# Kernel optimization log

Measured on AMD Instinct MI355X. Metric: run time of the kernel, lower is better.

## Reference

```python
import jax, jax.numpy as jnp
import numpy as np

# Structure matrix S (n_hos*n_types=6, n_structures=8) and internal int_S (unused in forward)
S_MAT = np.array([[1,0,1,0,0,1,0,1],[0,1,0,1,1,0,0,0],[1,1,0,0,0,0,1,0],[0,0,1,1,0,1,0,0],[0,1,1,0,1,0,0,1],[1,0,0,0,1,0,1,0]], dtype=np.float32)
CONTROL_STRENGTH = 10.0  # self.control_strength
PDHG_ITERS = 150         # fixed-iteration batched primal-dual LP solver
BATCH = 32768
N_STRUCT = 8
N_COMBO = 6


def setup_inputs() -> dict:
    key = jax.random.key(0)
    ks = jax.random.split(key, 9)
    X = jax.random.uniform(ks[0], (BATCH, 2, 3), jnp.float32)  # nonnegative bids
    def lin(k, fan_in, fan_out):
        return jax.random.normal(k, (fan_in, fan_out), jnp.float32) * (1.0 / np.sqrt(fan_in))
    W1 = lin(ks[1], 6, 20);  b1 = jnp.zeros((20,), jnp.float32)
    W2 = lin(ks[2], 20, 20); b2 = jnp.zeros((20,), jnp.float32)
    W3 = lin(ks[3], 20, 20); b3 = jnp.zeros((20,), jnp.float32)
    W4 = lin(ks[4], 20, 8);  b4 = jnp.zeros((8,), jnp.float32)
    S = jnp.asarray(S_MAT)
    return {"X": X, "W1": W1, "b1": b1, "W2": W2, "b2": b2, "W3": W3, "b3": b3,
            "W4": W4, "b4": b4, "S": S, "batch_size": BATCH}


def _mlp(Z, W1, b1, W2, b2, W3, b3, W4, b4):
    h = jnp.tanh(Z @ W1 + b1)
    h = jnp.tanh(h @ W2 + b2)
    h = jnp.tanh(h @ W3 + b3)
    return h @ W4 + b4  # [B, 8]


def _batched_lp(S, z, bvec):
    """Solve, per batch row: max 1'x - c*||x - z||_2  s.t. x>=0, S x <= b.
    Equivalent polytope A x <= b' with A=[S; -I], b'=[b; 0]; solved with PDHG.
    z, bvec: [B, 8], [B, 6]."""
    B = z.shape[0]
    A = jnp.concatenate([S, -jnp.eye(N_STRUCT, dtype=S.dtype)], axis=0)  # [14, 8]
    bfull = jnp.concatenate([bvec, jnp.zeros((B, N_STRUCT), bvec.dtype)], axis=1)  # [B, 14]
    L = jnp.linalg.norm(A)  # Frobenius norm upper-bounds spectral norm
    tau = 1.0 / L
    sigma = 1.0 / L

    def prox_g(v):
        # prox of g(x) = -1'x + c||x - z||_2 (w = ones): shift by tau*w then shrink toward z
        u = v + tau
        d = u - z
        n = jnp.linalg.norm(d, axis=-1, keepdims=True)
        scale = jnp.maximum(0.0, 1.0 - tau * CONTROL_STRENGTH / jnp.maximum(n, 1e-12))
        return z + scale * d

    x0 = jnp.maximum(z, 0.0)
    y0 = jnp.zeros((B, N_COMBO + N_STRUCT), z.dtype)

    def step(carry, _):
        x, xbar, y = carry
        y = jnp.maximum(0.0, y + sigma * (xbar @ A.T - bfull))  # dual ascent + proj >= 0
        x_new = prox_g(x - tau * (y @ A))                        # primal prox step
        return (x_new, 2.0 * x_new - x, y), None

    (x, _, _), _ = jax.lax.scan(step, (x0, x0, y0), None, length=PDHG_ITERS)
    return x


def reference(X, W1, b1, W2, b2, W3, b3, W4, b4, S, batch_size):
    B = X.shape[0]
    Z = X.reshape(B, N_COMBO)              # view(-1, n_hos*n_types)
    z = _mlp(Z, W1, b1, W2, b2, W3, b3, W4, b4)  # neural_net_forward -> [B, 8]
    x1 = _batched_lp(S, z, Z)              # linear_program_forward (W = ones)
    return x1
```

## Files before the change

### kernel.cpp

```cpp
#include <hip/hip_runtime.h>
#include <math.h>


#define N_ITERS 150
typedef float f2 __attribute__((ext_vector_type(2)));
typedef float f4 __attribute__((ext_vector_type(4)));

__device__ __forceinline__ float fast_tanh(float a) {
    float e = __expf(2.0f * a);
    return 1.0f - 2.0f * __builtin_amdgcn_rcpf(e + 1.0f);
}

__device__ __forceinline__ float dpp_swap(float v) {
    union { float f; int i; } u;
    u.f = v;
    u.i = __builtin_amdgcn_update_dpp(0, u.i, 0xB1, 0xF, 0xF, true);
    return u.f;
}

__global__ void __launch_bounds__(64)
__attribute__((amdgpu_waves_per_eu(1, 1)))
matchnet_kernel(
    const float* __restrict__ X,
    const float* __restrict__ W1, const float* __restrict__ b1,
    const float* __restrict__ W2, const float* __restrict__ b2,
    const float* __restrict__ W3, const float* __restrict__ b3,
    const float* __restrict__ W4, const float* __restrict__ b4,
    float* __restrict__ out, int B)
{
    __shared__ alignas(16) float tW1[160], tW2[400], tW3[400], tW4[160];
    __shared__ alignas(16) float sb1[20], sb2[20], sb3[20], sb4[8];
    {
        int tid = threadIdx.x;
        for (int idx = tid; idx < 120; idx += 64) { int i = idx / 20, j = idx % 20; tW1[j * 8 + i] = W1[idx]; }
        for (int idx = tid; idx < 400; idx += 64) { int i = idx / 20, j = idx % 20; tW2[j * 20 + i] = W2[idx]; }
        for (int idx = tid; idx < 400; idx += 64) { int i = idx / 20, j = idx % 20; tW3[j * 20 + i] = W3[idx]; }
        for (int idx = tid; idx < 160; idx += 64) { int i = idx / 8,  k = idx % 8;  tW4[k * 20 + i] = W4[idx]; }
        if (tid < 20) { sb1[tid] = b1[tid]; sb2[tid] = b2[tid]; sb3[tid] = b3[tid]; }
        if (tid < 8) sb4[tid] = b4[tid];
    }
    __syncthreads();

    int gidx = blockIdx.x * blockDim.x + threadIdx.x;
    int row = gidx >> 1;
    if (row >= B) return;
    const bool isOdd = (gidx & 1) != 0;
    const int jb = isOdd ? 10 : 0;
    const int kb = isOdd ? 4 : 0;

    float bb0 = X[row * 6 + 0], bb1 = X[row * 6 + 1], bb2 = X[row * 6 + 2];
    float bb3 = X[row * 6 + 3], bb4 = X[row * 6 + 4], bb5 = X[row * 6 + 5];

    float hA[10], hB[10];
    {
        float acc[10];
        const f2* bv = (const f2*)&sb1[jb];
        #pragma unroll
        for (int p = 0; p < 5; p++) { f2 b = bv[p]; acc[2 * p] = b.x; acc[2 * p + 1] = b.y; }
        #pragma unroll
        for (int n = 0; n < 10; n++) {
            int j = jb + n;
            f4 w0 = *(const f4*)&tW1[j * 8];
            f2 w1 = *(const f2*)&tW1[j * 8 + 4];
            float a = acc[n];
            a = fmaf(bb0, w0.x, a); a = fmaf(bb1, w0.y, a); a = fmaf(bb2, w0.z, a);
            a = fmaf(bb3, w0.w, a); a = fmaf(bb4, w1.x, a); a = fmaf(bb5, w1.y, a);
            acc[n] = fast_tanh(a);
        }
        #pragma unroll
        for (int n = 0; n < 10; n++) {
            float t = dpp_swap(acc[n]);
            hA[n] = isOdd ? t : acc[n];
            hB[n] = isOdd ? acc[n] : t;
        }
    }
    #pragma unroll
    for (int layer = 0; layer < 2; layer++) {
        const float* tw = layer ? tW3 : tW2;
        const float* sb = layer ? sb3 : sb2;
        float acc[10];
        const f2* bv = (const f2*)&sb[jb];
        #pragma unroll
        for (int p = 0; p < 5; p++) { f2 b = bv[p]; acc[2 * p] = b.x; acc[2 * p + 1] = b.y; }
        #pragma unroll
        for (int n = 0; n < 10; n++) {
            int j = jb + n;
            const f4* w = (const f4*)&tw[j * 20];
            f4 w0 = w[0], w1 = w[1], w2 = w[2], w3 = w[3], w4 = w[4];
            float a = acc[n];
            a = fmaf(hA[0], w0.x, a); a = fmaf(hA[1], w0.y, a);
            a = fmaf(hA[2], w0.z, a); a = fmaf(hA[3], w0.w, a);
            a = fmaf(hA[4], w1.x, a); a = fmaf(hA[5], w1.y, a);
            a = fmaf(hA[6], w1.z, a); a = fmaf(hA[7], w1.w, a);
            a = fmaf(hA[8], w2.x, a); a = fmaf(hA[9], w2.y, a);
            a = fmaf(hB[0], w2.z, a); a = fmaf(hB[1], w2.w, a);
            a = fmaf(hB[2], w3.x, a); a = fmaf(hB[3], w3.y, a);
            a = fmaf(hB[4], w3.z, a); a = fmaf(hB[5], w3.w, a);
            a = fmaf(hB[6], w4.x, a); a = fmaf(hB[7], w4.y, a);
            a = fmaf(hB[8], w4.z, a); a = fmaf(hB[9], w4.w, a);
            acc[n] = fast_tanh(a);
        }
        #pragma unroll
        for (int n = 0; n < 10; n++) {
            float t = dpp_swap(acc[n]);
            hA[n] = isOdd ? t : acc[n];
            hB[n] = isOdd ? acc[n] : t;
        }
    }
    float oz0, oz1, oz2, oz3;
    {
        f4 b = *(const f4*)&sb4[kb];
        float acc[4] = {b.x, b.y, b.z, b.w};
        #pragma unroll
        for (int n = 0; n < 4; n++) {
            int k = kb + n;
            const f4* w = (const f4*)&tW4[k * 20];
            f4 w0 = w[0], w1 = w[1], w2 = w[2], w3 = w[3], w4 = w[4];
            float a = acc[n];
            a = fmaf(hA[0], w0.x, a); a = fmaf(hA[1], w0.y, a);
            a = fmaf(hA[2], w0.z, a); a = fmaf(hA[3], w0.w, a);
            a = fmaf(hA[4], w1.x, a); a = fmaf(hA[5], w1.y, a);
            a = fmaf(hA[6], w1.z, a); a = fmaf(hA[7], w1.w, a);
            a = fmaf(hA[8], w2.x, a); a = fmaf(hA[9], w2.y, a);
            a = fmaf(hB[0], w2.z, a); a = fmaf(hB[1], w2.w, a);
            a = fmaf(hB[2], w3.x, a); a = fmaf(hB[3], w3.y, a);
            a = fmaf(hB[4], w3.z, a); a = fmaf(hB[5], w3.w, a);
            a = fmaf(hB[6], w4.x, a); a = fmaf(hB[7], w4.y, a);
            a = fmaf(hB[8], w4.z, a); a = fmaf(hB[9], w4.w, a);
            acc[n] = a;
        }
        oz0 = acc[0]; oz1 = acc[1]; oz2 = acc[2]; oz3 = acc[3];
    }

    const float tau  = 0.18898223650461363f;
    const float c    = 0.03571428571428571f;
    const float tauC = 1.8898223650461363f;

    float ot0 = tau - oz0, ot1 = tau - oz1, ot2 = tau - oz2, ot3 = tau - oz3;
    float oTI0 = ot0, oTI1 = ot1, oTI2 = ot2, oTI3 = ot3;

    float ox0 = fmaxf(oz0, 0.f), ox1 = fmaxf(oz1, 0.f);
    float ox2 = fmaxf(oz2, 0.f), ox3 = fmaxf(oz3, 0.f);
    float oxb0 = ox0, oxb1 = ox1, oxb2 = ox2, oxb3 = ox3;

    float cb0 = c * bb0, cb1 = c * bb1, cb2 = c * bb2;
    float cb3 = c * bb3, cb4 = c * bb4, cb5 = c * bb5;
    float cbq0 = isOdd ? cb4 : cb0;
    float cbq1 = isOdd ? cb3 : cb2;
    float cbq2 = isOdd ? cb5 : cb1;
    float Yq0 = 0.f, Yq1 = 0.f, Yq2 = 0.f;

    #pragma unroll 1
    for (int it = 0; it < N_ITERS; it++) {
        float rxb0 = dpp_swap(oxb0), rxb1 = dpp_swap(oxb1);
        float rxb2 = dpp_swap(oxb2), rxb3 = dpp_swap(oxb3);

        float op_a = oxb0 + rxb1;
        float op_b = oxb2 + rxb3;
        float op_c = oxb3 + rxb2;
        float op_d = isOdd ? op_c : op_b;
        float sq0  = op_a + op_d;
        float op_e = oxb1 + rxb2;
        float op_f = isOdd ? rxb3 : oxb0;
        float sq1  = op_e + op_f;
        float op_g = oxb1 + oxb3;
        float op_h = oxb0 + oxb2;
        float op_i = isOdd ? op_h : op_g;
        float sq2  = op_i + rxb0;

        Yq0 = fmaxf(0.f, fmaf(c, sq0, Yq0) - cbq0);
        Yq1 = fmaxf(0.f, fmaf(c, sq1, Yq1) - cbq1);
        Yq2 = fmaxf(0.f, fmaf(c, sq2, Yq2) - cbq2);

        float rY0 = dpp_swap(Yq0), rY1 = dpp_swap(Yq1), rY2 = dpp_swap(Yq2);

        float op_j = Yq0 + rY2;
        float op_k = isOdd ? Yq2 : Yq1;
        float colq0 = op_j + op_k;
        float op_l = Yq1 + rY0;
        float op_p = isOdd ? 0.f : Yq2;
        float colq1 = op_l + op_p;
        float op_m = Yq0 + rY0;
        float op_n = rY1 + Yq2;
        float op_o = op_m + rY1;
        float colq2 = isOdd ? op_n : op_o;
        float colq3 = isOdd ? op_m : op_n;

        oTI0 = fmaxf(ot0, fmaf(-c, oxb0, oTI0));
        oTI1 = fmaxf(ot1, fmaf(-c, oxb1, oTI1));
        oTI2 = fmaxf(ot2, fmaf(-c, oxb2, oTI2));
        oTI3 = fmaxf(ot3, fmaf(-c, oxb3, oTI3));

        float od0 = (ox0 + oTI0) - colq0;
        float od1 = (ox1 + oTI1) - colq1;
        float od2 = (ox2 + oTI2) - colq2;
        float od3 = (ox3 + oTI3) - colq3;

        float nl = od0 * od0;
        nl = fmaf(od1, od1, nl);
        nl = fmaf(od2, od2, nl);
        nl = fmaf(od3, od3, nl);
        float rn = dpp_swap(nl);
        float nsq = nl + rn;

        float rs = __builtin_amdgcn_rsqf(nsq);
        float scale = fmaxf(0.f, fmaf(-tauC, rs, 1.f));

        float xn0 = fmaf(scale, od0, oz0);
        float xn1 = fmaf(scale, od1, oz1);
        float xn2 = fmaf(scale, od2, oz2);
        float xn3 = fmaf(scale, od3, oz3);
        oxb0 = fmaf(2.f, xn0, -ox0); ox0 = xn0;
        oxb1 = fmaf(2.f, xn1, -ox1); ox1 = xn1;
        oxb2 = fmaf(2.f, xn2, -ox2); ox2 = xn2;
        oxb3 = fmaf(2.f, xn3, -ox3); ox3 = xn3;
    }

    float4* out4 = (float4*)out;
    out4[gidx] = make_float4(ox0, ox1, ox2, ox3);
}

extern "C" void kernel_launch(void* const* d_in, const int* in_sizes, int n_in,
                              void* d_out, int out_size, void* d_ws, size_t ws_size,
                              hipStream_t stream) {
    const float* X  = (const float*)d_in[0];
    const float* W1 = (const float*)d_in[1];
    const float* b1 = (const float*)d_in[2];
    const float* W2 = (const float*)d_in[3];
    const float* b2 = (const float*)d_in[4];
    const float* W3 = (const float*)d_in[5];
    const float* b3 = (const float*)d_in[6];
    const float* W4 = (const float*)d_in[7];
    const float* b4 = (const float*)d_in[8];
    float* out = (float*)d_out;

    int B = in_sizes[0] / 6;
    const int block = 64;
    long long threads = (long long)B * 2;
    int grid = (int)((threads + block - 1) / block);
    hipLaunchKernelGGL(matchnet_kernel, dim3(grid), dim3(block), 0, stream,
                       X, W1, b1, W2, b2, W3, b3, W4, b4, out, B);
}
```

Baseline: 101.6 us.

## Process one batch row per thread instead of splitting rows across lane pairs

Each thread now computes the full MLP and the full 8-variable PDHG iteration for one row, removing the DPP lane-swap exchanges and the row split across paired lanes. This eliminates the cross-lane communication and the redundant selects. In exchange it halves the number of threads and waves, so each thread carries twice the per-iteration work and fewer SIMDs are occupied.

```diff
diff --git a/kernel.cpp b/kernel.cpp
--- a/kernel.cpp
+++ b/kernel.cpp
@@ -9,13 +9,6 @@
 __device__ __forceinline__ float fast_tanh(float a) {
     float e = __expf(2.0f * a);
     return 1.0f - 2.0f * __builtin_amdgcn_rcpf(e + 1.0f);
-}
-
-__device__ __forceinline__ float dpp_swap(float v) {
-    union { float f; int i; } u;
-    u.f = v;
-    u.i = __builtin_amdgcn_update_dpp(0, u.i, 0xB1, 0xF, 0xF, true);
-    return u.f;
 }
 
 __global__ void __launch_bounds__(64)
@@ -41,183 +34,146 @@
     }
     __syncthreads();
 
-    int gidx = blockIdx.x * blockDim.x + threadIdx.x;
-    int row = gidx >> 1;
+    int row = blockIdx.x * blockDim.x + threadIdx.x;
     if (row >= B) return;
-    const bool isOdd = (gidx & 1) != 0;
-    const int jb = isOdd ? 10 : 0;
-    const int kb = isOdd ? 4 : 0;
 
-    float bb0 = X[row * 6 + 0], bb1 = X[row * 6 + 1], bb2 = X[row * 6 + 2];
-    float bb3 = X[row * 6 + 3], bb4 = X[row * 6 + 4], bb5 = X[row * 6 + 5];
+    const f2* xp = (const f2*)(X + row * 6);
+    f2 x01 = xp[0], x23 = xp[1], x45 = xp[2];
+    float bb0 = x01.x, bb1 = x01.y, bb2 = x23.x;
+    float bb3 = x23.y, bb4 = x45.x, bb5 = x45.y;
 
-    float hA[10], hB[10];
-    {
-        float acc[10];
-        const f2* bv = (const f2*)&sb1[jb];
-        #pragma unroll
-        for (int p = 0; p < 5; p++) { f2 b = bv[p]; acc[2 * p] = b.x; acc[2 * p + 1] = b.y; }
-        #pragma unroll
-        for (int n = 0; n < 10; n++) {
-            int j = jb + n;
-            f4 w0 = *(const f4*)&tW1[j * 8];
-            f2 w1 = *(const f2*)&tW1[j * 8 + 4];
-            float a = acc[n];
-            a = fmaf(bb0, w0.x, a); a = fmaf(bb1, w0.y, a); a = fmaf(bb2, w0.z, a);
-            a = fmaf(bb3, w0.w, a); a = fmaf(bb4, w1.x, a); a = fmaf(bb5, w1.y, a);
-            acc[n] = fast_tanh(a);
-        }
-        #pragma unroll
-        for (int n = 0; n < 10; n++) {
-            float t = dpp_swap(acc[n]);
-            hA[n] = isOdd ? t : acc[n];
-            hB[n] = isOdd ? acc[n] : t;
-        }
+    float h[20];
+    #pragma unroll
+    for (int j = 0; j < 20; j++) {
+        f4 w0 = *(const f4*)&tW1[j * 8];
+        f2 w1 = *(const f2*)&tW1[j * 8 + 4];
+        float a = sb1[j];
+        a = fmaf(bb0, w0.x, a); a = fmaf(bb1, w0.y, a); a = fmaf(bb2, w0.z, a);
+        a = fmaf(bb3, w0.w, a); a = fmaf(bb4, w1.x, a); a = fmaf(bb5, w1.y, a);
+        h[j] = fast_tanh(a);
     }
     #pragma unroll
     for (int layer = 0; layer < 2; layer++) {
         const float* tw = layer ? tW3 : tW2;
         const float* sb = layer ? sb3 : sb2;
-        float acc[10];
-        const f2* bv = (const f2*)&sb[jb];
+        float hn[20];
         #pragma unroll
-        for (int p = 0; p < 5; p++) { f2 b = bv[p]; acc[2 * p] = b.x; acc[2 * p + 1] = b.y; }
-        #pragma unroll
-        for (int n = 0; n < 10; n++) {
-            int j = jb + n;
+        for (int j = 0; j < 20; j++) {
             const f4* w = (const f4*)&tw[j * 20];
             f4 w0 = w[0], w1 = w[1], w2 = w[2], w3 = w[3], w4 = w[4];
-            float a = acc[n];
-            a = fmaf(hA[0], w0.x, a); a = fmaf(hA[1], w0.y, a);
-            a = fmaf(hA[2], w0.z, a); a = fmaf(hA[3], w0.w, a);
-            a = fmaf(hA[4], w1.x, a); a = fmaf(hA[5], w1.y, a);
-            a = fmaf(hA[6], w1.z, a); a = fmaf(hA[7], w1.w, a);
-            a = fmaf(hA[8], w2.x, a); a = fmaf(hA[9], w2.y, a);
-            a = fmaf(hB[0], w2.z, a); a = fmaf(hB[1], w2.w, a);
-            a = fmaf(hB[2], w3.x, a); a = fmaf(hB[3], w3.y, a);
-            a = fmaf(hB[4], w3.z, a); a = fmaf(hB[5], w3.w, a);
-            a = fmaf(hB[6], w4.x, a); a = fmaf(hB[7], w4.y, a);
-            a = fmaf(hB[8], w4.z, a); a = fmaf(hB[9], w4.w, a);
-            acc[n] = fast_tanh(a);
+            float a = sb[j];
+            a = fmaf(h[0],  w0.x, a); a = fmaf(h[1],  w0.y, a);
+            a = fmaf(h[2],  w0.z, a); a = fmaf(h[3],  w0.w, a);
+            a = fmaf(h[4],  w1.x, a); a = fmaf(h[5],  w1.y, a);
+            a = fmaf(h[6],  w1.z, a); a = fmaf(h[7],  w1.w, a);
+            a = fmaf(h[8],  w2.x, a); a = fmaf(h[9],  w2.y, a);
+            a = fmaf(h[10], w2.z, a); a = fmaf(h[11], w2.w, a);
+            a = fmaf(h[12], w3.x, a); a = fmaf(h[13], w3.y, a);
+            a = fmaf(h[14], w3.z, a); a = fmaf(h[15], w3.w, a);
+            a = fmaf(h[16], w4.x, a); a = fmaf(h[17], w4.y, a);
+            a = fmaf(h[18], w4.z, a); a = fmaf(h[19], w4.w, a);
+            hn[j] = fast_tanh(a);
         }
         #pragma unroll
-        for (int n = 0; n < 10; n++) {
-            float t = dpp_swap(acc[n]);
-            hA[n] = isOdd ? t : acc[n];
-            hB[n] = isOdd ? acc[n] : t;
-        }
+        for (int j = 0; j < 20; j++) h[j] = hn[j];
     }
-    float oz0, oz1, oz2, oz3;
-    {
-        f4 b = *(const f4*)&sb4[kb];
-        float acc[4] = {b.x, b.y, b.z, b.w};
-        #pragma unroll
-        for (int n = 0; n < 4; n++) {
-            int k = kb + n;
-            const f4* w = (const f4*)&tW4[k * 20];
-            f4 w0 = w[0], w1 = w[1], w2 = w[2], w3 = w[3], w4 = w[4];
-            float a = acc[n];
-            a = fmaf(hA[0], w0.x, a); a = fmaf(hA[1], w0.y, a);
-            a = fmaf(hA[2], w0.z, a); a = fmaf(hA[3], w0.w, a);
-            a = fmaf(hA[4], w1.x, a); a = fmaf(hA[5], w1.y, a);
-            a = fmaf(hA[6], w1.z, a); a = fmaf(hA[7], w1.w, a);
-            a = fmaf(hA[8], w2.x, a); a = fmaf(hA[9], w2.y, a);
-            a = fmaf(hB[0], w2.z, a); a = fmaf(hB[1], w2.w, a);
-            a = fmaf(hB[2], w3.x, a); a = fmaf(hB[3], w3.y, a);
-            a = fmaf(hB[4], w3.z, a); a = fmaf(hB[5], w3.w, a);
-            a = fmaf(hB[6], w4.x, a); a = fmaf(hB[7], w4.y, a);
-            a = fmaf(hB[8], w4.z, a); a = fmaf(hB[9], w4.w, a);
-            acc[n] = a;
-        }
-        oz0 = acc[0]; oz1 = acc[1]; oz2 = acc[2]; oz3 = acc[3];
+    float z[8];
+    #pragma unroll
+    for (int k = 0; k < 8; k++) {
+        const f4* w = (const f4*)&tW4[k * 20];
+        f4 w0 = w[0], w1 = w[1], w2 = w[2], w3 = w[3], w4 = w[4];
+        float a = sb4[k];
+        a = fmaf(h[0],  w0.x, a); a = fmaf(h[1],  w0.y, a);
+        a = fmaf(h[2],  w0.z, a); a = fmaf(h[3],  w0.w, a);
+        a = fmaf(h[4],  w1.x, a); a = fmaf(h[5],  w1.y, a);
+        a = fmaf(h[6],  w1.z, a); a = fmaf(h[7],  w1.w, a);
+        a = fmaf(h[8],  w2.x, a); a = fmaf(h[9],  w2.y, a);
+        a = fmaf(h[10], w2.z, a); a = fmaf(h[11], w2.w, a);
+        a = fmaf(h[12], w3.x, a); a = fmaf(h[13], w3.y, a);
+        a = fmaf(h[14], w3.z, a); a = fmaf(h[15], w3.w, a);
+        a = fmaf(h[16], w4.x, a); a = fmaf(h[17], w4.y, a);
+        a = fmaf(h[18], w4.z, a); a = fmaf(h[19], w4.w, a);
+        z[k] = a;
     }
 
     const float tau  = 0.18898223650461363f;
     const float c    = 0.03571428571428571f;
     const float tauC = 1.8898223650461363f;
 
-    float ot0 = tau - oz0, ot1 = tau - oz1, ot2 = tau - oz2, ot3 = tau - oz3;
-    float oTI0 = ot0, oTI1 = ot1, oTI2 = ot2, oTI3 = ot3;
-
-    float ox0 = fmaxf(oz0, 0.f), ox1 = fmaxf(oz1, 0.f);
-    float ox2 = fmaxf(oz2, 0.f), ox3 = fmaxf(oz3, 0.f);
-    float oxb0 = ox0, oxb1 = ox1, oxb2 = ox2, oxb3 = ox3;
-
+    float oz[8], ot[8], TI[8], x[8], xb[8];
+    #pragma unroll
+    for (int i = 0; i < 8; i++) {
+        oz[i] = z[i];
+        ot[i] = tau - z[i];
+        TI[i] = ot[i];
+        x[i]  = fmaxf(z[i], 0.f);
+        xb[i] = x[i];
+    }
     float cb0 = c * bb0, cb1 = c * bb1, cb2 = c * bb2;
     float cb3 = c * bb3, cb4 = c * bb4, cb5 = c * bb5;
-    float cbq0 = isOdd ? cb4 : cb0;
-    float cbq1 = isOdd ? cb3 : cb2;
-    float cbq2 = isOdd ? cb5 : cb1;
-    float Yq0 = 0.f, Yq1 = 0.f, Yq2 = 0.f;
+    float Y0 = 0.f, Y1 = 0.f, Y2 = 0.f, Y3 = 0.f, Y4 = 0.f, Y5 = 0.f;
 
     #pragma unroll 1
     for (int it = 0; it < N_ITERS; it++) {
-        float rxb0 = dpp_swap(oxb0), rxb1 = dpp_swap(oxb1);
-        float rxb2 = dpp_swap(oxb2), rxb3 = dpp_swap(oxb3);
+        float t27 = xb[2] + xb[7];
+        float s0 = (xb[0] + xb[5]) + t27;
+        float s4 = (xb[4] + xb[1]) + t27;
+        float s2 = (xb[1] + xb[6]) + xb[0];
+        float s3 = (xb[5] + xb[2]) + xb[3];
+        float s1 = (xb[1] + xb[3]) + xb[4];
+        float s5 = (xb[4] + xb[6]) + xb[0];
 
-        float op_a = oxb0 + rxb1;
-        float op_b = oxb2 + rxb3;
-        float op_c = oxb3 + rxb2;
-        float op_d = isOdd ? op_c : op_b;
-        float sq0  = op_a + op_d;
-        float op_e = oxb1 + rxb2;
-        float op_f = isOdd ? rxb3 : oxb0;
-        float sq1  = op_e + op_f;
-        float op_g = oxb1 + oxb3;
-        float op_h = oxb0 + oxb2;
-        float op_i = isOdd ? op_h : op_g;
-        float sq2  = op_i + rxb0;
+        Y0 = fmaxf(0.f, fmaf(c, s0, Y0) - cb0);
+        Y2 = fmaxf(0.f, fmaf(c, s2, Y2) - cb2);
+        Y1 = fmaxf(0.f, fmaf(c, s1, Y1) - cb1);
+        Y4 = fmaxf(0.f, fmaf(c, s4, Y4) - cb4);
+        Y3 = fmaxf(0.f, fmaf(c, s3, Y3) - cb3);
+        Y5 = fmaxf(0.f, fmaf(c, s5, Y5) - cb5);
 
-        Yq0 = fmaxf(0.f, fmaf(c, sq0, Yq0) - cbq0);
-        Yq1 = fmaxf(0.f, fmaf(c, sq1, Yq1) - cbq1);
-        Yq2 = fmaxf(0.f, fmaf(c, sq2, Yq2) - cbq2);
+        float u04 = Y0 + Y4;
+        float col[8];
+        col[0] = (Y0 + Y5) + Y2;
+        col[1] = (Y2 + Y4) + Y1;
+        col[2] = u04 + Y3;
+        col[3] = Y3 + Y1;
+        col[4] = (Y4 + Y1) + Y5;
+        col[5] = Y3 + Y0;
+        col[6] = Y2 + Y5;
+        col[7] = u04;
 
-        float rY0 = dpp_swap(Yq0), rY1 = dpp_swap(Yq1), rY2 = dpp_swap(Yq2);
+        #pragma unroll
+        for (int i = 0; i < 8; i++)
+            TI[i] = fmaxf(ot[i], fmaf(-c, xb[i], TI[i]));
 
-        float op_j = Yq0 + rY2;
-        float op_k = isOdd ? Yq2 : Yq1;
-        float colq0 = op_j + op_k;
-        float op_l = Yq1 + rY0;
-        float op_p = isOdd ? 0.f : Yq2;
-        float colq1 = op_l + op_p;
-        float op_m = Yq0 + rY0;
-        float op_n = rY1 + Yq2;
-        float op_o = op_m + rY1;
-        float colq2 = isOdd ? op_n : op_o;
-        float colq3 = isOdd ? op_m : op_n;
+        float d[8];
+        #pragma unroll
+        for (int i = 0; i < 8; i++)
+            d[i] = (x[i] + TI[i]) - col[i];
 
-        oTI0 = fmaxf(ot0, fmaf(-c, oxb0, oTI0));
-        oTI1 = fmaxf(ot1, fmaf(-c, oxb1, oTI1));
-        oTI2 = fmaxf(ot2, fmaf(-c, oxb2, oTI2));
-        oTI3 = fmaxf(ot3, fmaf(-c, oxb3, oTI3));
-
-        float od0 = (ox0 + oTI0) - colq0;
-        float od1 = (ox1 + oTI1) - colq1;
-        float od2 = (ox2 + oTI2) - colq2;
-        float od3 = (ox3 + oTI3) - colq3;
-
-        float nl = od0 * od0;
-        nl = fmaf(od1, od1, nl);
-        nl = fmaf(od2, od2, nl);
-        nl = fmaf(od3, od3, nl);
-        float rn = dpp_swap(nl);
-        float nsq = nl + rn;
+        float nlA = d[0] * d[0];
+        nlA = fmaf(d[1], d[1], nlA);
+        nlA = fmaf(d[2], d[2], nlA);
+        nlA = fmaf(d[3], d[3], nlA);
+        float nlB = d[4] * d[4];
+        nlB = fmaf(d[5], d[5], nlB);
+        nlB = fmaf(d[6], d[6], nlB);
+        nlB = fmaf(d[7], d[7], nlB);
+        float nsq = nlA + nlB;
 
         float rs = __builtin_amdgcn_rsqf(nsq);
         float scale = fmaxf(0.f, fmaf(-tauC, rs, 1.f));
 
-        float xn0 = fmaf(scale, od0, oz0);
-        float xn1 = fmaf(scale, od1, oz1);
-        float xn2 = fmaf(scale, od2, oz2);
-        float xn3 = fmaf(scale, od3, oz3);
-        oxb0 = fmaf(2.f, xn0, -ox0); ox0 = xn0;
-        oxb1 = fmaf(2.f, xn1, -ox1); ox1 = xn1;
-        oxb2 = fmaf(2.f, xn2, -ox2); ox2 = xn2;
-        oxb3 = fmaf(2.f, xn3, -ox3); ox3 = xn3;
+        #pragma unroll
+        for (int i = 0; i < 8; i++) {
+            float xn = fmaf(scale, d[i], oz[i]);
+            xb[i] = fmaf(2.f, xn, -x[i]);
+            x[i]  = xn;
+        }
     }
 
     float4* out4 = (float4*)out;
-    out4[gidx] = make_float4(ox0, ox1, ox2, ox3);
+    out4[row * 2]     = make_float4(x[0], x[1], x[2], x[3]);
+    out4[row * 2 + 1] = make_float4(x[4], x[5], x[6], x[7]);
 }
 
 extern "C" void kernel_launch(void* const* d_in, const int* in_sizes, int n_in,
@@ -236,8 +192,7 @@
 
     int B = in_sizes[0] / 6;
     const int block = 64;
-    long long threads = (long long)B * 2;
-    int grid = (int)((threads + block - 1) / block);
+    int grid = (B + block - 1) / block;
     hipLaunchKernelGGL(matchnet_kernel, dim3(grid), dim3(block), 0, stream,
                        X, W1, b1, W2, b2, W3, b3, W4, b4, out, B);
 }
```

Result: slower. 115.9 us (+14.1%).
